# Optimization experiments

Measured on AMD Instinct MI355X. Metric: run time of the kernel, lower is better.

Reference implementation:

```python
import jax, jax.numpy as jnp
import numpy as np

D_MODEL = 1024
N_HEADS = 16
D_K = D_MODEL // N_HEADS


def setup_inputs() -> dict:
    key = jax.random.key(0)
    ks = jax.random.split(key, 8)
    B, S = 2, 2048
    scale = np.sqrt(2.0 / D_MODEL).astype(np.float32)
    return {
        "query": jax.random.normal(ks[0], (B, S, D_MODEL), jnp.float32),
        "key": jax.random.normal(ks[1], (B, S, D_MODEL), jnp.float32),
        "value": jax.random.normal(ks[2], (B, S, D_MODEL), jnp.float32),
        "mask": jax.random.randint(ks[3], (B, 1, S), 0, 2).astype(bool),
        "W_Q": jax.random.normal(ks[4], (D_MODEL, D_MODEL), jnp.float32) * scale,
        "W_K": jax.random.normal(ks[5], (D_MODEL, D_MODEL), jnp.float32) * scale,
        "W_V": jax.random.normal(ks[6], (D_MODEL, D_MODEL), jnp.float32) * scale,
        "W_O": jax.random.normal(ks[7], (D_MODEL, D_MODEL), jnp.float32) * scale,
    }


def reference(query, key, value, mask, W_Q, W_K, W_V, W_O):
    B, Sq, _ = query.shape
    # projections: [B, S, d_model] @ [d_model, d_model]
    def split_heads(x):  # -> [B, H, S, d_k]
        return x.reshape(B, -1, N_HEADS, D_K).transpose(0, 2, 1, 3)
    Q = split_heads(query @ W_Q)
    K = split_heads(key @ W_K)
    V = split_heads(value @ W_V)
    # scores: [B, H, Sq, Sk]
    scores = jnp.einsum("bhqd,bhkd->bhqk", Q, K) / jnp.sqrt(jnp.float32(D_K))
    m = mask[:, None, :, :]  # [B,1,1,Sk]
    scores = jnp.where(m, -jnp.inf, scores)
    attn = jax.nn.softmax(scores, axis=-1)
    out = jnp.einsum("bhqk,bhkd->bhqd", attn, V)  # [B,H,Sq,d_k]
    out = out.transpose(0, 2, 1, 3).reshape(B, Sq, D_MODEL)
    return out @ W_O
```

## Files before the change

### kernel.cpp

```cpp
#include <hip/hip_runtime.h>
#include <hip/hip_bf16.h>
#include <stdint.h>

#define DM  1024
#define SEQ 2048
#define NB  2
#define NH  16
#define DKH 64
#define SCL 0.18033688f

typedef unsigned short u16;
typedef __attribute__((ext_vector_type(8))) short short8;
typedef __attribute__((ext_vector_type(4))) float f32x4;

#define MFMA(a,b,c) __builtin_amdgcn_mfma_f32_16x16x32_bf16((a),(b),(c),0,0,0)

__device__ __forceinline__ void async_g2l16(const void* g, void* l) {
  __builtin_amdgcn_global_load_lds(
      (const __attribute__((address_space(1))) uint32_t*)g,
      (__attribute__((address_space(3))) uint32_t*)l, 16, 0, 0);
}

__device__ __forceinline__ u16 f2bf(float f) {
  uint32_t u = __builtin_bit_cast(uint32_t, f);
  u += 0x7fffu + ((u >> 16) & 1u);
  return (u16)(u >> 16);
}

__device__ __forceinline__ short8 lds_sw(const char* base, int row, int cb) {
  return *(const short8*)(base + row * 128 + (cb ^ ((row & 7) << 4)));
}

__global__ __launch_bounds__(256) void conv3(
    const float* __restrict__ a0, const float* __restrict__ a1,
    const float* __restrict__ a2, u16* __restrict__ out) {
  const int z = blockIdx.z;
  const float* A = (z == 0) ? a0 : (z == 1) ? a1 : a2;
  u16* O = out + (size_t)z * NB * SEQ * DM;
  const size_t i = (size_t)blockIdx.x * 256 + threadIdx.x;
  const float4 a = ((const float4*)A)[i * 2];
  const float4 b = ((const float4*)A)[i * 2 + 1];
  u16 v[8] __attribute__((aligned(16)));
  v[0] = f2bf(a.x); v[1] = f2bf(a.y); v[2] = f2bf(a.z); v[3] = f2bf(a.w);
  v[4] = f2bf(b.x); v[5] = f2bf(b.y); v[6] = f2bf(b.z); v[7] = f2bf(b.w);
  *(uint4*)(O + i * 8) = *(uint4*)v;
}

__global__ __launch_bounds__(256) void transpose4(
    const float* __restrict__ w0, const float* __restrict__ w1,
    const float* __restrict__ w2, const float* __restrict__ w3,
    u16* __restrict__ o0, u16* __restrict__ o1,
    u16* __restrict__ o2, u16* __restrict__ o3) {
  __shared__ u16 tile[64][65];
  const int z = blockIdx.z;
  const float* W = (z == 0) ? w0 : (z == 1) ? w1 : (z == 2) ? w2 : w3;
  u16* O         = (z == 0) ? o0 : (z == 1) ? o1 : (z == 2) ? o2 : o3;
  const int k0 = blockIdx.x * 64, n0 = blockIdx.y * 64;
  const int t = threadIdx.x;
  const int r = t >> 2, cg = (t & 3) * 16;

  const float* src = W + (size_t)(k0 + r) * DM + n0 + cg;
#pragma unroll
  for (int j = 0; j < 4; ++j) {
    const float4 a = ((const float4*)src)[j];
    tile[r][cg + j * 4 + 0] = f2bf(a.x);
    tile[r][cg + j * 4 + 1] = f2bf(a.y);
    tile[r][cg + j * 4 + 2] = f2bf(a.z);
    tile[r][cg + j * 4 + 3] = f2bf(a.w);
  }
  __syncthreads();
  u16 u[16] __attribute__((aligned(16)));
#pragma unroll
  for (int j = 0; j < 16; ++j) u[j] = tile[cg + j][r];
  u16* dst = O + (size_t)(n0 + r) * DM + k0 + cg;
  *(uint4*)&dst[0] = *(uint4*)&u[0];
  *(uint4*)&dst[8] = *(uint4*)&u[8];
}

__global__ __launch_bounds__(256) void mask_scan(
    const int* __restrict__ mask, int* __restrict__ idx, int* __restrict__ nkv) {
  __shared__ int cnt[256];
  const int b = blockIdx.x, t = threadIdx.x;
  const int* mp = mask + b * SEQ + t * 8;
  int m[8], c = 0;
#pragma unroll
  for (int j = 0; j < 8; ++j) { m[j] = mp[j]; c += (m[j] == 0); }
  cnt[t] = c;
  __syncthreads();
  for (int off = 1; off < 256; off <<= 1) {
    int v = 0;
    if (t >= off) v = cnt[t - off];
    __syncthreads();
    if (t >= off) cnt[t] += v;
    __syncthreads();
  }
  int base = cnt[t] - c;
  int* ip = idx + b * SEQ;
#pragma unroll
  for (int j = 0; j < 8; ++j)
    if (m[j] == 0) ip[base++] = t * 8 + j;
  const int total = cnt[255];
  if (t == 0) nkv[b] = total;
  for (int p = total + t; p < SEQ; p += 256) ip[p] = 0;
}

__global__ __launch_bounds__(256) void vtransg(
    const u16* __restrict__ Vin, const int* __restrict__ idx, u16* __restrict__ Vt) {
  __shared__ u16 tile[64][65];
  const int posT = blockIdx.x;
  const int dmT  = blockIdx.y;
  const int b    = blockIdx.z;
  const int t = threadIdx.x;
  const int r = t >> 2, cg = (t & 3) * 16;
  const int srow = idx[b * SEQ + posT * 64 + r];
  const u16* src = Vin + ((size_t)b * SEQ + srow) * DM + dmT * 64 + cg;
  u16 v[16] __attribute__((aligned(16)));
  *(uint4*)&v[0] = *(const uint4*)src;
  *(uint4*)&v[8] = *(const uint4*)(src + 8);
#pragma unroll
  for (int j = 0; j < 16; ++j) tile[r][cg + j] = v[j];
  __syncthreads();
  u16 u[16] __attribute__((aligned(16)));
#pragma unroll
  for (int j = 0; j < 16; ++j) u[j] = tile[cg + j][r];
  u16* dst = Vt + ((size_t)b * DM + dmT * 64 + r) * SEQ + posT * 64 + cg;
  *(uint4*)&dst[0] = *(uint4*)&u[0];
  *(uint4*)&dst[8] = *(uint4*)&u[8];
}

template <int OUT_F32>
__device__ __forceinline__ void gemm128_body(
    const u16* __restrict__ A, const u16* __restrict__ Bt, void* __restrict__ Cv,
    int M, int N, int K, int bx, int by) {
  __shared__ u16 As[128 * 64];
  __shared__ u16 Bs[128 * 64];
  const int m0 = by * 128, n0 = bx * 128;
  const int t = threadIdx.x, w = t >> 6, l = t & 63;
  const int wr = w >> 1, wc = w & 1;
  const int frow = l & 15, fk8 = (l >> 4) * 8;
  f32x4 acc[4][4] = {};

  for (int k0 = 0; k0 < K; k0 += 64) {
#pragma unroll
    for (int i = 0; i < 4; ++i) {
      const int base = (i * 4 + w) * 1024;
      const int e = (base >> 1) + l * 8;
      const int row = e >> 6, col = e & 63;
      async_g2l16(A + (size_t)(m0 + row) * K + k0 + col, (char*)As + base);
      async_g2l16(Bt + (size_t)(n0 + row) * K + k0 + col, (char*)Bs + base);
    }
    __syncthreads();
#pragma unroll
    for (int kk = 0; kk < 2; ++kk) {
      short8 af[4], bf[4];
#pragma unroll
      for (int mi = 0; mi < 4; ++mi)
        af[mi] = *(const short8*)&As[(wr * 64 + mi * 16 + frow) * 64 + kk * 32 + fk8];
#pragma unroll
      for (int ni = 0; ni < 4; ++ni)
        bf[ni] = *(const short8*)&Bs[(wc * 64 + ni * 16 + frow) * 64 + kk * 32 + fk8];
#pragma unroll
      for (int mi = 0; mi < 4; ++mi)
#pragma unroll
        for (int ni = 0; ni < 4; ++ni)
          acc[mi][ni] = MFMA(af[mi], bf[ni], acc[mi][ni]);
    }
    __syncthreads();
  }

  const int crb = (l >> 4) * 4;
  for (int mi = 0; mi < 4; ++mi)
    for (int ni = 0; ni < 4; ++ni)
#pragma unroll
      for (int r = 0; r < 4; ++r) {
        const int row = m0 + wr * 64 + mi * 16 + crb + r;
        const int col = n0 + wc * 64 + ni * 16 + frow;
        if (OUT_F32) ((float*)Cv)[(size_t)row * N + col] = acc[mi][ni][r];
        else         ((u16*)Cv)[(size_t)row * N + col] = f2bf(acc[mi][ni][r]);
      }
}

__global__ __launch_bounds__(256) void gemm_qkv(
    const u16* __restrict__ xin, const u16* __restrict__ wt, u16* __restrict__ out) {
  const int z = blockIdx.z;
  gemm128_body<0>(xin + (size_t)z * NB * SEQ * DM, wt + (size_t)z * DM * DM,
                  out + (size_t)z * NB * SEQ * DM,
                  NB * SEQ, DM, DM, blockIdx.x, blockIdx.y);
}

__global__ __launch_bounds__(256) void gemm_out(
    const u16* __restrict__ A, const u16* __restrict__ Bt, float* __restrict__ C) {
  gemm128_body<1>(A, Bt, C, NB * SEQ, DM, DM, blockIdx.x, blockIdx.y);
}

__global__ __launch_bounds__(256) void attn(
    const u16* __restrict__ Q, const u16* __restrict__ Kp,
    const u16* __restrict__ Vtc, const int* __restrict__ idx,
    const int* __restrict__ nkv, u16* __restrict__ O) {
  __shared__ uint4 ldsv[40960 / 16];
  char* lds = (char*)ldsv;
  char* KB = lds;
  char* VB = lds + 16384;
  char* PB = lds + 32768;

  const int bid = blockIdx.x;
  const int qt = bid & 31;
  const int h  = (bid >> 5) & 15;
  const int b  = bid >> 9;
  const int t = threadIdx.x, w = t >> 6, l = t & 63;
  const int frow = l & 15, fk8 = (l >> 4) * 8, crb = (l >> 4) * 4;
  const size_t tok0 = (size_t)b * SEQ;
  const int q0 = qt * 64 + w * 16;
  const int hc = h * DKH;
  char* PW = PB + w * 2048;

  const int nk = nkv[b];
  const int nt = (nk + 63) >> 6;

  const int T0 = w * 2048 + l * 16;
  const int T1 = T0 + 1024;
  const int r0 = T0 >> 7, r1 = T1 >> 7;
  const int c0 = (T0 & 127) ^ ((r0 & 7) << 4);
  const int c1 = (T1 & 127) ^ ((r1 & 7) << 4);
  const u16* Kg = Kp + tok0 * DM + hc;
  const u16* Vg = Vtc + ((size_t)b * DM + hc) * SEQ;
  const int* ib = idx + b * SEQ;

  short8 qf[2];
#pragma unroll
  for (int ks = 0; ks < 2; ++ks)
    qf[ks] = *(const short8*)(Q + (tok0 + q0 + frow) * DM + hc + ks * 32 + fk8);

  const short ONE = 0x3F80;
  const short8 ONES = {ONE, ONE, ONE, ONE, ONE, ONE, ONE, ONE};

  f32x4 o[4] = {};
  f32x4 ol = {};
  float negm[4] = {-8.f, -8.f, -8.f, -8.f};

  u16* pwa[4][4];
#pragma unroll
  for (int n = 0; n < 4; ++n)
#pragma unroll
    for (int r = 0; r < 4; ++r)
      pwa[n][r] = (u16*)(PW + (crb + r) * 128 +
                         ((((n * 16 + frow) * 2)) ^ (((crb + r) & 7) << 4)));

  int ia0, ia1;
  if (nt > 0) {
    ia0 = ib[r0]; ia1 = ib[r1];
    async_g2l16((const char*)(Kg + (size_t)ia0 * DM) + c0, KB + w * 2048);
    async_g2l16((const char*)(Kg + (size_t)ia1 * DM) + c1, KB + w * 2048 + 1024);
    async_g2l16((const char*)(Vg + (size_t)r0 * SEQ) + c0, VB + w * 2048);
    async_g2l16((const char*)(Vg + (size_t)r1 * SEQ) + c1, VB + w * 2048 + 1024);
    ia0 = ib[(64 + r0) & 2047]; ia1 = ib[(64 + r1) & 2047];
  }

  int cur = 0;
  for (int it = 0; it < nt; ++it) {
    const int kv0 = it * 64;
    asm volatile("s_waitcnt vmcnt(0)" ::: "memory");
    __syncthreads();
    if (it + 1 < nt) {
      char* kd = KB + (cur ^ 1) * 8192 + w * 2048;
      char* vd = VB + (cur ^ 1) * 8192 + w * 2048;
      async_g2l16((const char*)(Kg + (size_t)ia0 * DM) + c0, kd);
      async_g2l16((const char*)(Kg + (size_t)ia1 * DM) + c1, kd + 1024);
      async_g2l16((const char*)(Vg + (size_t)r0 * SEQ + kv0 + 64) + c0, vd);
      async_g2l16((const char*)(Vg + (size_t)r1 * SEQ + kv0 + 64) + c1, vd + 1024);
      ia0 = ib[((it + 2) * 64 + r0) & 2047];
      ia1 = ib[((it + 2) * 64 + r1) & 2047];
    }
    const char* Kt = KB + cur * 8192;
    const char* Vt = VB + cur * 8192;

    f32x4 s[4];
#pragma unroll
    for (int n = 0; n < 4; ++n) {
      short8 kf0 = lds_sw(Kt, n * 16 + frow, fk8 * 2);
      short8 kf1 = lds_sw(Kt, n * 16 + frow, 64 + fk8 * 2);
      f32x4 a = {};
      a = MFMA(qf[0], kf0, a);
      a = MFMA(qf[1], kf1, a);
      s[n] = a;
    }
#pragma unroll
    for (int n = 0; n < 4; ++n)
#pragma unroll
      for (int r = 0; r < 4; ++r)
        s[n][r] = __builtin_fmaf(s[n][r], SCL, negm[r]);

    if (it == nt - 1) {
#pragma unroll
      for (int n = 0; n < 4; ++n) {
        const bool valid = (kv0 + n * 16 + frow) < nk;
#pragma unroll
        for (int r = 0; r < 4; ++r)
          s[n][r] = valid ? s[n][r] : -1e30f;
      }
    }

    float lm = fmaxf(fmaxf(fmaxf(s[0][0], s[0][1]), fmaxf(s[0][2], s[0][3])),
                     fmaxf(fmaxf(s[1][0], s[1][1]), fmaxf(s[1][2], s[1][3])));
    lm = fmaxf(lm, fmaxf(fmaxf(s[2][0], s[2][1]), fmaxf(s[2][2], s[2][3])));
    lm = fmaxf(lm, fmaxf(fmaxf(s[3][0], s[3][1]), fmaxf(s[3][2], s[3][3])));
    if (__any(lm > 8.0f)) {
#pragma unroll
      for (int r = 0; r < 4; ++r) {
        float mx = fmaxf(fmaxf(s[0][r], s[1][r]), fmaxf(s[2][r], s[3][r]));
        mx = fmaxf(mx, __shfl_xor(mx, 1));
        mx = fmaxf(mx, __shfl_xor(mx, 2));
        mx = fmaxf(mx, __shfl_xor(mx, 4));
        mx = fmaxf(mx, __shfl_xor(mx, 8));
        const float d = fmaxf(mx, 0.f);
        const float al = exp2f(-d);
        negm[r] -= d;
        ol[r] *= al;
#pragma unroll
        for (int dd = 0; dd < 4; ++dd) o[dd][r] *= al;
#pragma unroll
        for (int n = 0; n < 4; ++n) s[n][r] -= d;
      }
    }

#pragma unroll
    for (int n = 0; n < 4; ++n)
#pragma unroll
      for (int r = 0; r < 4; ++r) {
        const float p = exp2f(s[n][r]);
        *pwa[n][r] = (u16)(__builtin_bit_cast(uint32_t, p) >> 16);
      }
    asm volatile("s_waitcnt lgkmcnt(0)" ::: "memory");
    __builtin_amdgcn_sched_barrier(0);

    short8 pa0 = lds_sw(PW, frow, fk8 * 2);
    short8 pa1 = lds_sw(PW, frow, 64 + fk8 * 2);
    ol = MFMA(pa1, ONES, MFMA(pa0, ONES, ol));
#pragma unroll
    for (int d = 0; d < 4; ++d) {
      short8 vf0 = lds_sw(Vt, d * 16 + frow, fk8 * 2);
      short8 vf1 = lds_sw(Vt, d * 16 + frow, 64 + fk8 * 2);
      o[d] = MFMA(pa1, vf1, MFMA(pa0, vf0, o[d]));
    }
    cur ^= 1;
  }

#pragma unroll
  for (int r = 0; r < 4; ++r) {
    const float den = ol[r];
    const float inv = den > 0.f ? 1.f / den : 0.f;
#pragma unroll
    for (int d = 0; d < 4; ++d)
      O[(tok0 + q0 + crb + r) * DM + hc + d * 16 + frow] = f2bf(o[d][r] * inv);
  }
}

extern "C" void kernel_launch(void* const* d_in, const int* in_sizes, int n_in,
                              void* d_out, int out_size, void* d_ws, size_t ws_size,
                              hipStream_t stream) {
  const float* query = (const float*)d_in[0];
  const float* key_  = (const float*)d_in[1];
  const float* value = (const float*)d_in[2];
  const int* mask    = (const int*)d_in[3];
  const float* wq = (const float*)d_in[4];
  const float* wk = (const float*)d_in[5];
  const float* wv = (const float*)d_in[6];
  const float* wo = (const float*)d_in[7];
  float* out = (float*)d_out;
  char* ws = (char*)d_ws;

  u16* wt_qkv = (u16*)(ws);
  u16* wt_o   = (u16*)(ws + (6u << 20));
  u16* xin    = (u16*)(ws + (8u << 20));
  u16* vtc    = (u16*)(ws + (8u << 20));
  u16* attn_o = (u16*)(ws + (16u << 20));
  u16* qkv    = (u16*)(ws + (32u << 20));
  int* idx    = (int*)(ws + (56u << 20));
  int* nkv    = (int*)(ws + (56u << 20) + 16384);

  transpose4<<<dim3(16, 16, 4), 256, 0, stream>>>(
      wq, wk, wv, wo,
      wt_qkv, wt_qkv + (size_t)DM * DM, wt_qkv + (size_t)2 * DM * DM, wt_o);

  conv3<<<dim3(2048, 1, 3), 256, 0, stream>>>(query, key_, value, xin);

  mask_scan<<<dim3(NB), 256, 0, stream>>>(mask, idx, nkv);

  gemm_qkv<<<dim3(DM / 128, (NB * SEQ) / 128, 3), 256, 0, stream>>>(
      xin, wt_qkv, qkv);

  vtransg<<<dim3(32, 16, NB), 256, 0, stream>>>(
      qkv + (size_t)2 * NB * SEQ * DM, idx, vtc);

  attn<<<dim3(NB * NH * (SEQ / 64)), 256, 0, stream>>>(
      qkv, qkv + (size_t)NB * SEQ * DM, vtc, idx, nkv, attn_o);

  gemm_out<<<dim3(DM / 128, (NB * SEQ) / 128), 256, 0, stream>>>(
      attn_o, wt_o, out);
}
```

Measured before the change: 238.0 us.

## Fuse prep kernels, compact K, triple-buffer attention with 512-thread blocks

Merges weight transpose, input conversion and mask scan into one prep launch, and folds the V transpose and a new K compaction into one kvprep launch. Attention now reads a pre-compacted K instead of gathering through idx, handles 128 queries per 512-thread block, and triple-buffers K/V tiles with partial vmcnt waits so loads overlap compute. Block-index swizzles are added to the GEMMs and attention to improve cache locality. The costs are an extra K copy, more LDS per block, and possibly lower occupancy.

```diff
diff --git a/kernel.cpp b/kernel.cpp
--- a/kernel.cpp
+++ b/kernel.cpp
@@ -31,101 +31,112 @@
   return *(const short8*)(base + row * 128 + (cb ^ ((row & 7) << 4)));
 }
 
-__global__ __launch_bounds__(256) void conv3(
-    const float* __restrict__ a0, const float* __restrict__ a1,
-    const float* __restrict__ a2, u16* __restrict__ out) {
-  const int z = blockIdx.z;
-  const float* A = (z == 0) ? a0 : (z == 1) ? a1 : a2;
-  u16* O = out + (size_t)z * NB * SEQ * DM;
-  const size_t i = (size_t)blockIdx.x * 256 + threadIdx.x;
-  const float4 a = ((const float4*)A)[i * 2];
-  const float4 b = ((const float4*)A)[i * 2 + 1];
-  u16 v[8] __attribute__((aligned(16)));
-  v[0] = f2bf(a.x); v[1] = f2bf(a.y); v[2] = f2bf(a.z); v[3] = f2bf(a.w);
-  v[4] = f2bf(b.x); v[5] = f2bf(b.y); v[6] = f2bf(b.z); v[7] = f2bf(b.w);
-  *(uint4*)(O + i * 8) = *(uint4*)v;
-}
-
-__global__ __launch_bounds__(256) void transpose4(
+__global__ __launch_bounds__(256) void prep(
+    const float* __restrict__ query, const float* __restrict__ key_,
+    const float* __restrict__ value, const int* __restrict__ mask,
     const float* __restrict__ w0, const float* __restrict__ w1,
     const float* __restrict__ w2, const float* __restrict__ w3,
-    u16* __restrict__ o0, u16* __restrict__ o1,
-    u16* __restrict__ o2, u16* __restrict__ o3) {
-  __shared__ u16 tile[64][65];
-  const int z = blockIdx.z;
-  const float* W = (z == 0) ? w0 : (z == 1) ? w1 : (z == 2) ? w2 : w3;
-  u16* O         = (z == 0) ? o0 : (z == 1) ? o1 : (z == 2) ? o2 : o3;
-  const int k0 = blockIdx.x * 64, n0 = blockIdx.y * 64;
+    u16* __restrict__ xin, u16* __restrict__ wt_qkv, u16* __restrict__ wt_o,
+    int* __restrict__ idx, int* __restrict__ nkv) {
+  __shared__ char shm[8320];
+  const int bid = blockIdx.x;
   const int t = threadIdx.x;
-  const int r = t >> 2, cg = (t & 3) * 16;
-
-  const float* src = W + (size_t)(k0 + r) * DM + n0 + cg;
-#pragma unroll
-  for (int j = 0; j < 4; ++j) {
-    const float4 a = ((const float4*)src)[j];
-    tile[r][cg + j * 4 + 0] = f2bf(a.x);
-    tile[r][cg + j * 4 + 1] = f2bf(a.y);
-    tile[r][cg + j * 4 + 2] = f2bf(a.z);
-    tile[r][cg + j * 4 + 3] = f2bf(a.w);
+
+  if (bid < 1024) {
+    u16 (*tile)[65] = (u16(*)[65])shm;
+    const int z = bid >> 8, rem = bid & 255;
+    const float* W = (z == 0) ? w0 : (z == 1) ? w1 : (z == 2) ? w2 : w3;
+    u16* O = (z < 3) ? (wt_qkv + (size_t)z * DM * DM) : wt_o;
+    const int k0 = (rem & 15) * 64, n0 = (rem >> 4) * 64;
+    const int r = t >> 2, cg = (t & 3) * 16;
+    const float* src = W + (size_t)(k0 + r) * DM + n0 + cg;
+#pragma unroll
+    for (int j = 0; j < 4; ++j) {
+      const float4 a = ((const float4*)src)[j];
+      tile[r][cg + j * 4 + 0] = f2bf(a.x);
+      tile[r][cg + j * 4 + 1] = f2bf(a.y);
+      tile[r][cg + j * 4 + 2] = f2bf(a.z);
+      tile[r][cg + j * 4 + 3] = f2bf(a.w);
+    }
+    __syncthreads();
+    u16 u[16] __attribute__((aligned(16)));
+#pragma unroll
+    for (int j = 0; j < 16; ++j) u[j] = tile[cg + j][r];
+    u16* dst = O + (size_t)(n0 + r) * DM + k0 + cg;
+    *(uint4*)&dst[0] = *(uint4*)&u[0];
+    *(uint4*)&dst[8] = *(uint4*)&u[8];
+  } else if (bid < 7168) {
+    const int cb = bid - 1024;
+    const int z = cb >> 11;
+    const float* A = (z == 0) ? query : (z == 1) ? key_ : value;
+    u16* O = xin + (size_t)z * NB * SEQ * DM;
+    const size_t i = (size_t)(cb & 2047) * 256 + t;
+    const float4 a = ((const float4*)A)[i * 2];
+    const float4 b = ((const float4*)A)[i * 2 + 1];
+    u16 v[8] __attribute__((aligned(16)));
+    v[0] = f2bf(a.x); v[1] = f2bf(a.y); v[2] = f2bf(a.z); v[3] = f2bf(a.w);
+    v[4] = f2bf(b.x); v[5] = f2bf(b.y); v[6] = f2bf(b.z); v[7] = f2bf(b.w);
+    *(uint4*)(O + i * 8) = *(uint4*)v;
+  } else {
+    int* cnt = (int*)shm;
+    const int b = bid - 7168;
+    const int* mp = mask + b * SEQ + t * 8;
+    int m[8], c = 0;
+#pragma unroll
+    for (int j = 0; j < 8; ++j) { m[j] = mp[j]; c += (m[j] == 0); }
+    cnt[t] = c;
+    __syncthreads();
+    for (int off = 1; off < 256; off <<= 1) {
+      int v = 0;
+      if (t >= off) v = cnt[t - off];
+      __syncthreads();
+      if (t >= off) cnt[t] += v;
+      __syncthreads();
+    }
+    int base = cnt[t] - c;
+    int* ip = idx + b * SEQ;
+#pragma unroll
+    for (int j = 0; j < 8; ++j)
+      if (m[j] == 0) ip[base++] = t * 8 + j;
+    const int total = cnt[255];
+    if (t == 0) nkv[b] = total;
+    for (int p = total + t; p < SEQ; p += 256) ip[p] = 0;
   }
-  __syncthreads();
-  u16 u[16] __attribute__((aligned(16)));
-#pragma unroll
-  for (int j = 0; j < 16; ++j) u[j] = tile[cg + j][r];
-  u16* dst = O + (size_t)(n0 + r) * DM + k0 + cg;
-  *(uint4*)&dst[0] = *(uint4*)&u[0];
-  *(uint4*)&dst[8] = *(uint4*)&u[8];
-}
-
-__global__ __launch_bounds__(256) void mask_scan(
-    const int* __restrict__ mask, int* __restrict__ idx, int* __restrict__ nkv) {
-  __shared__ int cnt[256];
-  const int b = blockIdx.x, t = threadIdx.x;
-  const int* mp = mask + b * SEQ + t * 8;
-  int m[8], c = 0;
-#pragma unroll
-  for (int j = 0; j < 8; ++j) { m[j] = mp[j]; c += (m[j] == 0); }
-  cnt[t] = c;
-  __syncthreads();
-  for (int off = 1; off < 256; off <<= 1) {
-    int v = 0;
-    if (t >= off) v = cnt[t - off];
+}
+
+__global__ __launch_bounds__(256) void kvprep(
+    const u16* __restrict__ Kin, const u16* __restrict__ Vin,
+    const int* __restrict__ idx, u16* __restrict__ Kc, u16* __restrict__ Vt) {
+  const int bid = blockIdx.x;
+  const int t = threadIdx.x;
+  if (bid < 1024) {
+    __shared__ u16 tile[64][65];
+    const int posT = bid & 31, dmT = (bid >> 5) & 15, b = bid >> 9;
+    const int r = t >> 2, cg = (t & 3) * 16;
+    const int srow = idx[b * SEQ + posT * 64 + r];
+    const u16* src = Vin + ((size_t)b * SEQ + srow) * DM + dmT * 64 + cg;
+    u16 v[16] __attribute__((aligned(16)));
+    *(uint4*)&v[0] = *(const uint4*)src;
+    *(uint4*)&v[8] = *(const uint4*)(src + 8);
+#pragma unroll
+    for (int j = 0; j < 16; ++j) tile[r][cg + j] = v[j];
     __syncthreads();
-    if (t >= off) cnt[t] += v;
-    __syncthreads();
+    u16 u[16] __attribute__((aligned(16)));
+#pragma unroll
+    for (int j = 0; j < 16; ++j) u[j] = tile[cg + j][r];
+    u16* dst = Vt + ((size_t)b * DM + dmT * 64 + r) * SEQ + posT * 64 + cg;
+    *(uint4*)&dst[0] = *(uint4*)&u[0];
+    *(uint4*)&dst[8] = *(uint4*)&u[8];
+  } else {
+    const int kb = bid - 1024;
+    const int b = kb >> 6, rg = kb & 63;
+    const int r = rg * 32 + (t >> 3), chunk = t & 7;
+    const int srow = idx[b * SEQ + r];
+    const uint4* src = (const uint4*)(Kin + ((size_t)b * SEQ + srow) * DM) + chunk;
+    uint4* dst = (uint4*)(Kc + ((size_t)b * SEQ + r) * DM) + chunk;
+#pragma unroll
+    for (int j = 0; j < 16; ++j) dst[j * 8] = src[j * 8];
   }
-  int base = cnt[t] - c;
-  int* ip = idx + b * SEQ;
-#pragma unroll
-  for (int j = 0; j < 8; ++j)
-    if (m[j] == 0) ip[base++] = t * 8 + j;
-  const int total = cnt[255];
-  if (t == 0) nkv[b] = total;
-  for (int p = total + t; p < SEQ; p += 256) ip[p] = 0;
-}
-
-__global__ __launch_bounds__(256) void vtransg(
-    const u16* __restrict__ Vin, const int* __restrict__ idx, u16* __restrict__ Vt) {
-  __shared__ u16 tile[64][65];
-  const int posT = blockIdx.x;
-  const int dmT  = blockIdx.y;
-  const int b    = blockIdx.z;
-  const int t = threadIdx.x;
-  const int r = t >> 2, cg = (t & 3) * 16;
-  const int srow = idx[b * SEQ + posT * 64 + r];
-  const u16* src = Vin + ((size_t)b * SEQ + srow) * DM + dmT * 64 + cg;
-  u16 v[16] __attribute__((aligned(16)));
-  *(uint4*)&v[0] = *(const uint4*)src;
-  *(uint4*)&v[8] = *(const uint4*)(src + 8);
-#pragma unroll
-  for (int j = 0; j < 16; ++j) tile[r][cg + j] = v[j];
-  __syncthreads();
-  u16 u[16] __attribute__((aligned(16)));
-#pragma unroll
-  for (int j = 0; j < 16; ++j) u[j] = tile[cg + j][r];
-  u16* dst = Vt + ((size_t)b * DM + dmT * 64 + r) * SEQ + posT * 64 + cg;
-  *(uint4*)&dst[0] = *(uint4*)&u[0];
-  *(uint4*)&dst[8] = *(uint4*)&u[8];
 }
 
 template <int OUT_F32>
@@ -180,51 +191,54 @@
       }
 }
 
+__device__ __forceinline__ void swz256(int& bx, int& by) {
+  const int lin = by * 8 + bx;
+  const int s = (lin & 7) * 32 + (lin >> 3);
+  bx = s & 7; by = s >> 3;
+}
+
 __global__ __launch_bounds__(256) void gemm_qkv(
     const u16* __restrict__ xin, const u16* __restrict__ wt, u16* __restrict__ out) {
   const int z = blockIdx.z;
+  int bx = blockIdx.x, by = blockIdx.y;
+  swz256(bx, by);
   gemm128_body<0>(xin + (size_t)z * NB * SEQ * DM, wt + (size_t)z * DM * DM,
                   out + (size_t)z * NB * SEQ * DM,
-                  NB * SEQ, DM, DM, blockIdx.x, blockIdx.y);
+                  NB * SEQ, DM, DM, bx, by);
 }
 
 __global__ __launch_bounds__(256) void gemm_out(
     const u16* __restrict__ A, const u16* __restrict__ Bt, float* __restrict__ C) {
-  gemm128_body<1>(A, Bt, C, NB * SEQ, DM, DM, blockIdx.x, blockIdx.y);
-}
-
-__global__ __launch_bounds__(256) void attn(
-    const u16* __restrict__ Q, const u16* __restrict__ Kp,
-    const u16* __restrict__ Vtc, const int* __restrict__ idx,
-    const int* __restrict__ nkv, u16* __restrict__ O) {
-  __shared__ uint4 ldsv[40960 / 16];
+  int bx = blockIdx.x, by = blockIdx.y;
+  swz256(bx, by);
+  gemm128_body<1>(A, Bt, C, NB * SEQ, DM, DM, bx, by);
+}
+
+__global__ __launch_bounds__(512) void attn(
+    const u16* __restrict__ Q, const u16* __restrict__ Kc,
+    const u16* __restrict__ Vtc, const int* __restrict__ nkv,
+    u16* __restrict__ O) {
+  __shared__ uint4 ldsv[65536 / 16];
   char* lds = (char*)ldsv;
-  char* KB = lds;
-  char* VB = lds + 16384;
-  char* PB = lds + 32768;
 
   const int bid = blockIdx.x;
-  const int qt = bid & 31;
-  const int h  = (bid >> 5) & 15;
-  const int b  = bid >> 9;
+  const int swz = (bid & 7) * 64 + (bid >> 3);
+  const int qt = swz & 15, h = (swz >> 4) & 15, b = swz >> 8;
   const int t = threadIdx.x, w = t >> 6, l = t & 63;
   const int frow = l & 15, fk8 = (l >> 4) * 8, crb = (l >> 4) * 4;
   const size_t tok0 = (size_t)b * SEQ;
-  const int q0 = qt * 64 + w * 16;
+  const int q0 = qt * 128 + w * 16;
   const int hc = h * DKH;
-  char* PW = PB + w * 2048;
+  char* PW = lds + 49152 + w * 2048;
 
   const int nk = nkv[b];
   const int nt = (nk + 63) >> 6;
 
-  const int T0 = w * 2048 + l * 16;
-  const int T1 = T0 + 1024;
-  const int r0 = T0 >> 7, r1 = T1 >> 7;
+  const int T0 = w * 1024 + l * 16;
+  const int r0 = T0 >> 7;
   const int c0 = (T0 & 127) ^ ((r0 & 7) << 4);
-  const int c1 = (T1 & 127) ^ ((r1 & 7) << 4);
-  const u16* Kg = Kp + tok0 * DM + hc;
+  const u16* Kg = Kc + tok0 * DM + hc;
   const u16* Vg = Vtc + ((size_t)b * DM + hc) * SEQ;
-  const int* ib = idx + b * SEQ;
 
   short8 qf[2];
 #pragma unroll
@@ -238,41 +252,29 @@
   f32x4 ol = {};
   float negm[4] = {-8.f, -8.f, -8.f, -8.f};
 
-  u16* pwa[4][4];
-#pragma unroll
-  for (int n = 0; n < 4; ++n)
-#pragma unroll
-    for (int r = 0; r < 4; ++r)
-      pwa[n][r] = (u16*)(PW + (crb + r) * 128 +
-                         ((((n * 16 + frow) * 2)) ^ (((crb + r) & 7) << 4)));
-
-  int ia0, ia1;
-  if (nt > 0) {
-    ia0 = ib[r0]; ia1 = ib[r1];
-    async_g2l16((const char*)(Kg + (size_t)ia0 * DM) + c0, KB + w * 2048);
-    async_g2l16((const char*)(Kg + (size_t)ia1 * DM) + c1, KB + w * 2048 + 1024);
-    async_g2l16((const char*)(Vg + (size_t)r0 * SEQ) + c0, VB + w * 2048);
-    async_g2l16((const char*)(Vg + (size_t)r1 * SEQ) + c1, VB + w * 2048 + 1024);
-    ia0 = ib[(64 + r0) & 2047]; ia1 = ib[(64 + r1) & 2047];
-  }
-
-  int cur = 0;
+  char* kb0 = lds;          char* kb1 = lds + 8192;   char* kb2 = lds + 16384;
+  char* vb0 = lds + 24576;  char* vb1 = lds + 32768;  char* vb2 = lds + 40960;
+
+#define STAGE(tile, kd, vd)                                                    \
+  do {                                                                         \
+    const int kv_ = (tile) * 64;                                               \
+    async_g2l16((const char*)(Kg + (size_t)(kv_ + r0) * DM) + c0, (kd) + w * 1024); \
+    async_g2l16((const char*)(Vg + (size_t)r0 * SEQ + kv_) + c0, (vd) + w * 1024);  \
+  } while (0)
+
+  if (nt > 0) STAGE(0, kb0, vb0);
+  if (nt > 1) STAGE(1, kb1, vb1);
+
   for (int it = 0; it < nt; ++it) {
+    if (it + 1 < nt) { asm volatile("s_waitcnt vmcnt(2)" ::: "memory"); }
+    else             { asm volatile("s_waitcnt vmcnt(0)" ::: "memory"); }
+    __builtin_amdgcn_s_barrier();
+    __builtin_amdgcn_sched_barrier(0);
+    if (it + 2 < nt) STAGE(it + 2, kb2, vb2);
+
     const int kv0 = it * 64;
-    asm volatile("s_waitcnt vmcnt(0)" ::: "memory");
-    __syncthreads();
-    if (it + 1 < nt) {
-      char* kd = KB + (cur ^ 1) * 8192 + w * 2048;
-      char* vd = VB + (cur ^ 1) * 8192 + w * 2048;
-      async_g2l16((const char*)(Kg + (size_t)ia0 * DM) + c0, kd);
-      async_g2l16((const char*)(Kg + (size_t)ia1 * DM) + c1, kd + 1024);
-      async_g2l16((const char*)(Vg + (size_t)r0 * SEQ + kv0 + 64) + c0, vd);
-      async_g2l16((const char*)(Vg + (size_t)r1 * SEQ + kv0 + 64) + c1, vd + 1024);
-      ia0 = ib[((it + 2) * 64 + r0) & 2047];
-      ia1 = ib[((it + 2) * 64 + r1) & 2047];
-    }
-    const char* Kt = KB + cur * 8192;
-    const char* Vt = VB + cur * 8192;
+    const char* Kt = kb0;
+    const char* Vt = vb0;
 
     f32x4 s[4];
 #pragma unroll
@@ -328,7 +330,9 @@
 #pragma unroll
       for (int r = 0; r < 4; ++r) {
         const float p = exp2f(s[n][r]);
-        *pwa[n][r] = (u16)(__builtin_bit_cast(uint32_t, p) >> 16);
+        *(u16*)(PW + (crb + r) * 128 +
+                ((n * 32 + frow * 2) ^ (((crb + r) & 7) << 4))) =
+            (u16)(__builtin_bit_cast(uint32_t, p) >> 16);
       }
     asm volatile("s_waitcnt lgkmcnt(0)" ::: "memory");
     __builtin_amdgcn_sched_barrier(0);
@@ -342,8 +346,11 @@
       short8 vf1 = lds_sw(Vt, d * 16 + frow, 64 + fk8 * 2);
       o[d] = MFMA(pa1, vf1, MFMA(pa0, vf0, o[d]));
     }
-    cur ^= 1;
+
+    char* tk = kb0; kb0 = kb1; kb1 = kb2; kb2 = tk;
+    char* tv = vb0; vb0 = vb1; vb1 = vb2; vb2 = tv;
   }
+#undef STAGE
 
 #pragma unroll
   for (int r = 0; r < 4; ++r) {
@@ -374,26 +381,22 @@
   u16* xin    = (u16*)(ws + (8u << 20));
   u16* vtc    = (u16*)(ws + (8u << 20));
   u16* attn_o = (u16*)(ws + (16u << 20));
+  u16* kc     = (u16*)(ws + (24u << 20));
   u16* qkv    = (u16*)(ws + (32u << 20));
   int* idx    = (int*)(ws + (56u << 20));
   int* nkv    = (int*)(ws + (56u << 20) + 16384);
 
-  transpose4<<<dim3(16, 16, 4), 256, 0, stream>>>(
-      wq, wk, wv, wo,
-      wt_qkv, wt_qkv + (size_t)DM * DM, wt_qkv + (size_t)2 * DM * DM, wt_o);
-
-  conv3<<<dim3(2048, 1, 3), 256, 0, stream>>>(query, key_, value, xin);
-
-  mask_scan<<<dim3(NB), 256, 0, stream>>>(mask, idx, nkv);
+  prep<<<dim3(7170), 256, 0, stream>>>(
+      query, key_, value, mask, wq, wk, wv, wo, xin, wt_qkv, wt_o, idx, nkv);
 
   gemm_qkv<<<dim3(DM / 128, (NB * SEQ) / 128, 3), 256, 0, stream>>>(
       xin, wt_qkv, qkv);
 
-  vtransg<<<dim3(32, 16, NB), 256, 0, stream>>>(
-      qkv + (size_t)2 * NB * SEQ * DM, idx, vtc);
-
-  attn<<<dim3(NB * NH * (SEQ / 64)), 256, 0, stream>>>(
-      qkv, qkv + (size_t)NB * SEQ * DM, vtc, idx, nkv, attn_o);
+  kvprep<<<dim3(1152), 256, 0, stream>>>(
+      qkv + (size_t)NB * SEQ * DM, qkv + (size_t)2 * NB * SEQ * DM, idx, kc, vtc);
+
+  attn<<<dim3(NB * NH * (SEQ / 128)), 512, 0, stream>>>(
+      qkv, kc, vtc, nkv, attn_o);
 
   gemm_out<<<dim3(DM / 128, (NB * SEQ) / 128), 256, 0, stream>>>(
       attn_o, wt_o, out);
```

New measurement: 223.1 us. -6.2%, faster.
